# Optimization experiments

Measured on AMD Instinct MI355X. Metric: run time of the kernel, lower is better.

The kernel has to match this reference:

```python
import jax, jax.numpy as jnp
import numpy as np

MEAN = np.array([0.485, 0.456, 0.406], np.float32).reshape(1, 3, 1, 1)
STD = np.array([0.229, 0.224, 0.225], np.float32).reshape(1, 3, 1, 1)
BN_EPS = 1e-5


def _srm_kernels():
    """Standard SRM 30-filter 5x5 high-pass bank (Fridrich) -> [30,1,5,5]."""
    ks = []
    Z = lambda: np.zeros((5, 5), np.float32)
    D8 = [(-1, 0), (-1, 1), (0, 1), (1, 1), (1, 0), (1, -1), (0, -1), (-1, -1)]
    for dy, dx in D8:  # 8 first-order
        k = Z(); k[2, 2] = -1.0; k[2 + dy, 2 + dx] = 1.0; ks.append(k)
    for dy, dx in D8[:4]:  # 4 second-order
        k = Z(); k[2, 2] = -2.0; k[2 + dy, 2 + dx] = 1.0; k[2 - dy, 2 - dx] = 1.0
        ks.append(k / 2.0)
    for dy, dx in D8:  # 8 third-order
        k = Z()
        k[2 - dy, 2 - dx] = -1.0; k[2, 2] = 3.0
        k[2 + dy, 2 + dx] = -3.0; k[2 + 2 * dy, 2 + 2 * dx] = 1.0
        ks.append(k / 3.0)
    sq3 = np.array([[-1, 2, -1], [2, -4, 2], [-1, 2, -1]], np.float32) / 4.0
    k = Z(); k[1:4, 1:4] = sq3; ks.append(k)  # SQUARE 3x3
    sq5 = np.array([[-1, 2, -2, 2, -1], [2, -6, 8, -6, 2], [-2, 8, -12, 8, -2],
                    [2, -6, 8, -6, 2], [-1, 2, -2, 2, -1]], np.float32) / 12.0
    ks.append(sq5)  # SQUARE 5x5
    e3 = np.array([[-1, 2, -1], [2, -4, 2], [0, 0, 0]], np.float32) / 4.0
    for r in range(4):  # 4 EDGE 3x3
        k = Z(); k[1:4, 1:4] = np.rot90(e3, r); ks.append(k)
    e5 = np.array([[-1, 2, -2, 2, -1], [2, -6, 8, -6, 2], [-2, 8, -12, 8, -2],
                   [0, 0, 0, 0, 0], [0, 0, 0, 0, 0]], np.float32) / 4.0
    for r in range(4):  # 4 EDGE 5x5
        ks.append(np.rot90(e5, r).copy())
    return np.stack(ks)[:, None]  # [30,1,5,5]

SRM_K = jnp.asarray(_srm_kernels())
GAUSS_K = jnp.asarray((np.outer([1, 4, 6, 4, 1], [1, 4, 6, 4, 1]) / 256.0)
                      .astype(np.float32))[None, None]  # [1,1,5,5]
CFA_K = jnp.asarray((np.array([[0, 1, 0], [1, 0, 1], [0, 1, 0]], np.float32) / 4.0))[None, None]


def conv2d(x, w, b=None):
    y = jax.lax.conv_general_dilated(x, w, (1, 1), 'SAME',
                                     dimension_numbers=('NCHW', 'OIHW', 'NCHW'))
    if b is not None:
        y = y + b[None, :, None, None]
    return y


def batchnorm(x, g, b, m, v):
    inv = jax.lax.rsqrt(v + BN_EPS)
    return (x - m[None, :, None, None]) * (g * inv)[None, :, None, None] + b[None, :, None, None]


def extract_features(x):
    """Batched PRNU(1) + SRM(30) + CFA(1) feature maps -> [B,32,H,W]."""
    img = jnp.clip(x * STD + MEAN, 0.0, 1.0)  # denormalize
    gray = (0.299 * img[:, 0] + 0.587 * img[:, 1] + 0.114 * img[:, 2])[:, None]  # [B,1,H,W]
    prnu = gray - conv2d(gray, GAUSS_K)            # denoise-subtract noise residual
    srm = conv2d(gray, SRM_K)                       # [B,30,H,W]
    green = img[:, 1:2]
    cfa = green - conv2d(green, CFA_K)              # CFA interpolation residual
    return jnp.concatenate([prnu, srm, cfa], axis=1)  # [B,32,H,W]


def setup_inputs() -> dict:
    key = jax.random.key(0)
    ks = jax.random.split(key, 16)
    B, H, W = 16, 256, 256
    d = {"x": jax.random.normal(ks[0], (B, 3, H, W), jnp.float32)}
    cins = [32, 64, 64, 64]
    for i in range(4):
        cin, co = cins[i], 64
        scale = (2.0 / (cin * 9)) ** 0.5  # kaiming
        d[f"w{i+1}"] = jax.random.normal(ks[1 + i], (co, cin, 3, 3), jnp.float32) * scale
        d[f"b{i+1}"] = jnp.zeros((co,), jnp.float32)
        d[f"g{i+1}"] = jnp.ones((co,), jnp.float32)
        d[f"be{i+1}"] = jnp.zeros((co,), jnp.float32)
        d[f"m{i+1}"] = jax.random.normal(ks[5 + i], (co,), jnp.float32) * 0.1
        d[f"v{i+1}"] = jax.random.uniform(ks[9 + i], (co,), jnp.float32, 0.5, 1.5)
    return d


def reference(x, w1, b1, g1, be1, m1, v1, w2, b2, g2, be2, m2, v2,
              w3, b3, g3, be3, m3, v3, w4, b4, g4, be4, m4, v4):
    h = extract_features(x)
    for w, b, g, be, m, v in ((w1, b1, g1, be1, m1, v1), (w2, b2, g2, be2, m2, v2),
                              (w3, b3, g3, be3, m3, v3), (w4, b4, g4, be4, m4, v4)):
        h = jax.nn.relu(batchnorm(conv2d(h, w, b), g, be, m, v))
    return h  # [B,64,H,W]
```

## Files before the change

### kernel.cpp

```cpp
#include <hip/hip_runtime.h>
#include <hip/hip_bf16.h>
#include <cstddef>

#define B_ 16
#define H_ 256
#define W_ 256
#define HW_ (H_ * W_)
#define P_ 258


typedef _Float16 half8 __attribute__((ext_vector_type(8)));
typedef float floatx4 __attribute__((ext_vector_type(4)));

__device__ __forceinline__ void gload_lds16(void* lds, const void* g) {
  __builtin_amdgcn_global_load_lds(
      (const __attribute__((address_space(1))) unsigned int*)g,
      (__attribute__((address_space(3))) unsigned int*)lds, 16, 0, 0);
}

__global__ __launch_bounds__(256) void zero_border3(_Float16* __restrict__ f,
                                                    _Float16* __restrict__ a,
                                                    _Float16* __restrict__ bb) {
  int idx = blockIdx.x * 256 + threadIdx.x;
  int total = 16 * 20 * 1028;
  if (idx >= total) return;
  int p = idx % 1028;
  int rest = idx / 1028;
  int cg = rest % 20;
  int b = rest / 20;
  _Float16* buf;
  int ncg, c;
  if (cg < 4) { buf = f; ncg = 4; c = cg; }
  else if (cg < 12) { buf = a; ncg = 8; c = cg - 4; }
  else { buf = bb; ncg = 8; c = cg - 12; }
  int row, col;
  if (p < 258) { row = 0; col = p; }
  else if (p < 516) { row = 257; col = p - 258; }
  else if (p < 772) { row = p - 515; col = 0; }
  else { row = p - 771; col = 257; }
  *(floatx4*)&buf[(((size_t)(b * ncg + c) * P_ + row) * P_ + col) * 8] =
      (floatx4)0.f;
}

__global__ __launch_bounds__(256) void feat_kernel(const float* __restrict__ x,
                                                   _Float16* __restrict__ F) {
  __shared__ float sg[36][37];
  __shared__ float sgr[36][37];

  const int b = blockIdx.z;
  const int y0 = blockIdx.y * 32;
  const int x0 = blockIdx.x * 32;
  const float* xb = x + (size_t)b * 3 * HW_;

  for (int i = threadIdx.x; i < 36 * 36; i += 256) {
    int iy = i / 36, ix = i % 36;
    int gy = y0 + iy - 2, gx = x0 + ix - 2;
    float gray = 0.f, green = 0.f;
    if (gy >= 0 && gy < H_ && gx >= 0 && gx < W_) {
      int idx = gy * W_ + gx;
      float r = fminf(fmaxf(xb[idx] * 0.229f + 0.485f, 0.f), 1.f);
      float g = fminf(fmaxf(xb[idx + HW_] * 0.224f + 0.456f, 0.f), 1.f);
      float bl = fminf(fmaxf(xb[idx + 2 * HW_] * 0.225f + 0.406f, 0.f), 1.f);
      gray = 0.299f * r + 0.587f * g + 0.114f * bl;
      green = g;
    }
    sg[iy][ix] = gray;
    sgr[iy][ix] = green;
  }
  __syncthreads();

  for (int p = threadIdx.x; p < 32 * 32; p += 256) {
    const int py = p >> 5, px = p & 31;
    const int ly = py + 2, lx = px + 2;
#define G(dy, dx) sg[ly + (dy)][lx + (dx)]
    float f[32];
    const float c = G(0, 0);

    {
      const float ga[5] = {1.f, 4.f, 6.f, 4.f, 1.f};
      float s = 0.f;
#pragma unroll
      for (int i = 0; i < 5; i++) {
        float rs = 0.f;
#pragma unroll
        for (int j = 0; j < 5; j++) rs += ga[j] * G(i - 2, j - 2);
        s += ga[i] * rs;
      }
      f[0] = c - s * (1.0f / 256.0f);
    }

    const int dy8[8] = {-1, -1, 0, 1, 1, 1, 0, -1};
    const int dx8[8] = {0, 1, 1, 1, 0, -1, -1, -1};

#pragma unroll
    for (int k = 0; k < 8; k++) f[1 + k] = G(dy8[k], dx8[k]) - c;
#pragma unroll
    for (int k = 0; k < 4; k++)
      f[9 + k] = 0.5f * (G(dy8[k], dx8[k]) + G(-dy8[k], -dx8[k])) - c;
#pragma unroll
    for (int k = 0; k < 8; k++)
      f[13 + k] = (-G(-dy8[k], -dx8[k]) + 3.f * c - 3.f * G(dy8[k], dx8[k]) +
                   G(2 * dy8[k], 2 * dx8[k])) * (1.f / 3.f);

    {
      const float sq3[3][3] = {{-1, 2, -1}, {2, -4, 2}, {-1, 2, -1}};
      float s = 0.f;
#pragma unroll
      for (int i = 0; i < 3; i++)
#pragma unroll
        for (int j = 0; j < 3; j++) s += sq3[i][j] * G(i - 1, j - 1);
      f[21] = s * 0.25f;
    }
    {
      const float sq5[5][5] = {{-1, 2, -2, 2, -1},
                               {2, -6, 8, -6, 2},
                               {-2, 8, -12, 8, -2},
                               {2, -6, 8, -6, 2},
                               {-1, 2, -2, 2, -1}};
      float s = 0.f;
#pragma unroll
      for (int i = 0; i < 5; i++)
#pragma unroll
        for (int j = 0; j < 5; j++) s += sq5[i][j] * G(i - 2, j - 2);
      f[22] = s * (1.0f / 12.0f);
    }
    {
      const float e3[3][3] = {{-1, 2, -1}, {2, -4, 2}, {0, 0, 0}};
      float s0 = 0.f, s1 = 0.f, s2 = 0.f, s3 = 0.f;
#pragma unroll
      for (int i = 0; i < 3; i++)
#pragma unroll
        for (int j = 0; j < 3; j++) {
          float v = G(i - 1, j - 1);
          s0 += e3[i][j] * v;
          s1 += e3[j][2 - i] * v;
          s2 += e3[2 - i][2 - j] * v;
          s3 += e3[2 - j][i] * v;
        }
      f[23] = s0 * 0.25f;
      f[24] = s1 * 0.25f;
      f[25] = s2 * 0.25f;
      f[26] = s3 * 0.25f;
    }
    {
      const float e5[5][5] = {{-1, 2, -2, 2, -1},
                              {2, -6, 8, -6, 2},
                              {-2, 8, -12, 8, -2},
                              {0, 0, 0, 0, 0},
                              {0, 0, 0, 0, 0}};
      float s0 = 0.f, s1 = 0.f, s2 = 0.f, s3 = 0.f;
#pragma unroll
      for (int i = 0; i < 5; i++)
#pragma unroll
        for (int j = 0; j < 5; j++) {
          float v = G(i - 2, j - 2);
          s0 += e5[i][j] * v;
          s1 += e5[j][4 - i] * v;
          s2 += e5[4 - i][4 - j] * v;
          s3 += e5[4 - j][i] * v;
        }
      f[27] = s0 * 0.25f;
      f[28] = s1 * 0.25f;
      f[29] = s2 * 0.25f;
      f[30] = s3 * 0.25f;
    }
    {
      float gc = sgr[ly][lx];
      f[31] = gc - 0.25f * (sgr[ly - 1][lx] + sgr[ly][lx - 1] +
                            sgr[ly][lx + 1] + sgr[ly + 1][lx]);
    }
#undef G

    _Float16 h[32];
#pragma unroll
    for (int cc = 0; cc < 32; cc++) h[cc] = (_Float16)f[cc];
    const floatx4* src = (const floatx4*)h;
#pragma unroll
    for (int cg = 0; cg < 4; cg++)
      *(floatx4*)&F[(((size_t)(b * 4 + cg) * P_ + (y0 + py + 1)) * P_ +
                     (x0 + px + 1)) * 8] = src[cg];
  }
}

__global__ void wprep4_kernel(
    const float* __restrict__ w1, const float* __restrict__ b1,
    const float* __restrict__ g1, const float* __restrict__ be1,
    const float* __restrict__ m1, const float* __restrict__ v1,
    const float* __restrict__ w2, const float* __restrict__ b2,
    const float* __restrict__ g2, const float* __restrict__ be2,
    const float* __restrict__ m2, const float* __restrict__ v2,
    const float* __restrict__ w3, const float* __restrict__ b3,
    const float* __restrict__ g3, const float* __restrict__ be3,
    const float* __restrict__ m3, const float* __restrict__ v3,
    const float* __restrict__ w4, const float* __restrict__ b4,
    const float* __restrict__ g4, const float* __restrict__ be4,
    const float* __restrict__ m4, const float* __restrict__ v4,
    _Float16* __restrict__ wp1, _Float16* __restrict__ wp2,
    _Float16* __restrict__ wp3, _Float16* __restrict__ wp4,
    float* __restrict__ scsh) {
  const int layer = blockIdx.y;
  const float *w, *bias, *g, *be, *m, *v;
  _Float16* wp;
  int cin;
  switch (layer) {
    case 0: w = w1; bias = b1; g = g1; be = be1; m = m1; v = v1; wp = wp1; cin = 32; break;
    case 1: w = w2; bias = b2; g = g2; be = be2; m = m2; v = v2; wp = wp2; cin = 64; break;
    case 2: w = w3; bias = b3; g = g3; be = be3; m = m3; v = v3; wp = wp3; cin = 64; break;
    default: w = w4; bias = b4; g = g4; be = be4; m = m4; v = v4; wp = wp4; cin = 64; break;
  }
  int i = blockIdx.x * 256 + threadIdx.x;
  int total = cin * 9 * 64;
  if (i < total) {
    int j = i & 7;
    int co = (i >> 3) & 63;
    int rest = i >> 9;
    int t = rest % 9;
    int qc = rest / 9;
    int ci = qc * 8 + j;
    wp[i] = (_Float16)w[((size_t)co * cin + ci) * 9 + t];
  }
  if (i < 64) {
    float s = g[i] * rsqrtf(v[i] + 1e-5f);
    scsh[layer * 128 + i] = s;
    scsh[layer * 128 + 64 + i] = be[i] + (bias[i] - m[i]) * s;
  }
}

template <int CIN, bool FINAL>
__global__ __launch_bounds__(256, 2) void conv_mfma(
    const _Float16* __restrict__ in, const _Float16* __restrict__ wp,
    const float* __restrict__ sc, const float* __restrict__ sh,
    void* __restrict__ outv) {
  __shared__ char smem[42240];
  _Float16(*s_in)[10][66][8] = (_Float16(*)[10][66][8])smem;

  const int tid = threadIdx.x;
  const int b = blockIdx.z;
  const int y0 = blockIdx.y * 8;
  const int x0 = blockIdx.x * 64;
  const int wid = tid >> 6;
  const int lane = tid & 63;
  const int quad = lane >> 4;
  const int ln = lane & 15;

  floatx4 acc[8][4];
#pragma unroll
  for (int mt = 0; mt < 8; mt++)
#pragma unroll
    for (int nt = 0; nt < 4; nt++) acc[mt][nt] = (floatx4)0.f;

  for (int kc = 0; kc < CIN / 32; kc++) {
    __syncthreads();
    for (int i = tid; i < 2640; i += 256) {
      int q = i / 660, rem = i % 660;
      int row = rem / 66, col = rem % 66;
      gload_lds16(smem + i * 16,
                  &in[(((size_t)(b * (CIN / 8) + kc * 4 + q) * P_ +
                        (y0 + row)) * P_ + (x0 + col)) * 8]);
    }
    __syncthreads();

    const _Float16* wq = wp + (size_t)(kc * 4 + quad) * 9 * 512;
#pragma unroll
    for (int t = 0; t < 9; t++) {
      const int ty = t / 3, tx = t % 3;
      half8 a[8], bb[4];
#pragma unroll
      for (int nt = 0; nt < 4; nt++)
        bb[nt] = *(const half8*)&wq[t * 512 + (nt * 16 + ln) * 8];
#pragma unroll
      for (int mt = 0; mt < 8; mt++)
        a[mt] = *(const half8*)&s_in[quad][2 * wid + ty + (mt >> 2)]
                                    [(mt & 3) * 16 + ln + tx][0];
#pragma unroll
      for (int mt = 0; mt < 8; mt++)
#pragma unroll
        for (int nt = 0; nt < 4; nt++)
          acc[mt][nt] = __builtin_amdgcn_mfma_f32_16x16x32_f16(
              a[mt], bb[nt], acc[mt][nt], 0, 0, 0);
    }
  }

  if (FINAL) {
    float* out = (float*)outv;
#pragma unroll
    for (int nt = 0; nt < 4; nt++) {
      int co = nt * 16 + ln;
      float s = sc[co], t0 = sh[co];
#pragma unroll
      for (int mt = 0; mt < 8; mt++) {
        int y = y0 + 2 * wid + (mt >> 2);
        int xb = x0 + (mt & 3) * 16 + quad * 4;
        floatx4 vv;
#pragma unroll
        for (int r = 0; r < 4; r++) vv[r] = fmaxf(acc[mt][nt][r] * s + t0, 0.f);
        *(floatx4*)&out[(((size_t)b * 64 + co) * H_ + y) * W_ + xb] = vv;
      }
    }
  } else {
    __syncthreads();
    _Float16* s_out = (_Float16*)smem + wid * 5280;
    _Float16* out = (_Float16*)outv;
#pragma unroll
    for (int h = 0; h < 2; h++) {
      asm volatile("s_waitcnt lgkmcnt(0)" ::: "memory");
#pragma unroll
      for (int nt = 0; nt < 4; nt++) {
        int co = nt * 16 + ln;
        float s = sc[co], t0 = sh[co];
        int cog = co >> 3, clo = co & 7;
#pragma unroll
        for (int mt2 = 0; mt2 < 4; mt2++) {
          int lpix0 = mt2 * 16 + quad * 4;
#pragma unroll
          for (int r = 0; r < 4; r++) {
            int lpix = lpix0 + r;
            s_out[lpix * 64 + (((cog ^ (lpix & 7)) << 3) | clo)] =
                (_Float16)fmaxf(acc[h * 4 + mt2][nt][r] * s + t0, 0.f);
          }
        }
      }
      asm volatile("s_waitcnt lgkmcnt(0)" ::: "memory");
      int gy = y0 + 2 * wid + h + 1;
#pragma unroll
      for (int cog = 0; cog < 8; cog++) {
        *(floatx4*)&out[(((size_t)(b * 8 + cog) * P_ + gy) * P_ +
                         (x0 + lane + 1)) * 8] =
            *(const floatx4*)&s_out[lane * 64 + ((cog ^ (lane & 7)) << 3)];
      }
    }
  }
}

extern "C" void kernel_launch(void* const* d_in, const int* in_sizes, int n_in,
                              void* d_out, int out_size, void* d_ws,
                              size_t ws_size, hipStream_t stream) {
  const float* x = (const float*)d_in[0];
#define LAYER_PTRS(i)                                                       \
  const float* w##i = (const float*)d_in[1 + ((i)-1) * 6 + 0];              \
  const float* b##i = (const float*)d_in[1 + ((i)-1) * 6 + 1];              \
  const float* g##i = (const float*)d_in[1 + ((i)-1) * 6 + 2];              \
  const float* be##i = (const float*)d_in[1 + ((i)-1) * 6 + 3];             \
  const float* m##i = (const float*)d_in[1 + ((i)-1) * 6 + 4];              \
  const float* v##i = (const float*)d_in[1 + ((i)-1) * 6 + 5];
  LAYER_PTRS(1)
  LAYER_PTRS(2)
  LAYER_PTRS(3)
  LAYER_PTRS(4)
#undef LAYER_PTRS

  char* ws = (char*)d_ws;
  const size_t featB = (size_t)16 * 4 * P_ * P_ * 8 * 2;
  const size_t actB64 = (size_t)16 * 8 * P_ * P_ * 8 * 2;
  _Float16* feat = (_Float16*)ws;
  _Float16* actA = (_Float16*)(ws + featB);
  _Float16* actB = (_Float16*)(ws + featB + actB64);
  char* wbase = ws + featB + 2 * actB64;
  _Float16* wp1 = (_Float16*)(wbase);
  _Float16* wp2 = (_Float16*)(wbase + 36864);
  _Float16* wp3 = (_Float16*)(wbase + 36864 + 73728);
  _Float16* wp4 = (_Float16*)(wbase + 36864 + 2 * 73728);
  float* scsh = (float*)(wbase + 36864 + 3 * 73728);
  float *sc1 = scsh, *sh1 = scsh + 64;
  float *sc2 = scsh + 128, *sh2 = scsh + 192;
  float *sc3 = scsh + 256, *sh3 = scsh + 320;
  float *sc4 = scsh + 384, *sh4 = scsh + 448;

  dim3 wgrid(144, 4);
  wprep4_kernel<<<wgrid, 256, 0, stream>>>(
      w1, b1, g1, be1, m1, v1, w2, b2, g2, be2, m2, v2,
      w3, b3, g3, be3, m3, v3, w4, b4, g4, be4, m4, v4,
      wp1, wp2, wp3, wp4, scsh);

  zero_border3<<<1285, 256, 0, stream>>>(feat, actA, actB);

  dim3 fgrid(W_ / 32, H_ / 32, B_);
  feat_kernel<<<fgrid, 256, 0, stream>>>(x, feat);

  dim3 cgrid(W_ / 64, H_ / 8, B_);
  conv_mfma<32, false><<<cgrid, 256, 0, stream>>>(feat, wp1, sc1, sh1, actA);
  conv_mfma<64, false><<<cgrid, 256, 0, stream>>>(actA, wp2, sc2, sh2, actB);
  conv_mfma<64, false><<<cgrid, 256, 0, stream>>>(actB, wp3, sc3, sh3, actA);
  conv_mfma<64, true><<<cgrid, 256, 0, stream>>>(actA, wp4, sc4, sh4, d_out);
}
```

Measured before the change: 696.9 us.

## Double-buffer conv input tiles, retile to 16x32, prefetch weights and swizzle block order

The 3x3 MFMA conv kernel now uses 16x32-pixel tiles instead of 8x64, which shrinks halo overhead. Input channel chunks are staged into double-buffered LDS, so the next chunk's global-to-LDS copy overlaps the current chunk's MFMAs. Weights are repacked into a lane-contiguous layout and software-prefetched two taps ahead in alternating registers. A 1D grid with a remapped block index groups spatially neighbouring tiles across XCDs. The cost is more LDS per block (two buffers for the 64-channel layers), which may reduce occupancy.

```diff
diff --git a/kernel.cpp b/kernel.cpp
--- a/kernel.cpp
+++ b/kernel.cpp
@@ -212,11 +212,14 @@
   int total = cin * 9 * 64;
   if (i < total) {
     int j = i & 7;
-    int co = (i >> 3) & 63;
-    int rest = i >> 9;
+    int ln = (i >> 3) & 15;
+    int quad = (i >> 7) & 3;
+    int nt = (i >> 9) & 3;
+    int rest = i >> 11;
     int t = rest % 9;
-    int qc = rest / 9;
-    int ci = qc * 8 + j;
+    int kc = rest / 9;
+    int ci = (kc * 4 + quad) * 8 + j;
+    int co = nt * 16 + ln;
     wp[i] = (_Float16)w[((size_t)co * cin + ci) * 9 + t];
   }
   if (i < 64) {
@@ -231,13 +234,18 @@
     const _Float16* __restrict__ in, const _Float16* __restrict__ wp,
     const float* __restrict__ sc, const float* __restrict__ sh,
     void* __restrict__ outv) {
-  __shared__ char smem[42240];
-  _Float16(*s_in)[10][66][8] = (_Float16(*)[10][66][8])smem;
+  constexpr int NP = CIN / 8;
+  constexpr int NKC = CIN / 32;
+  constexpr int IN_BYTES = 4 * 18 * 34 * 8 * 2;
+  __shared__ char smem[NKC * IN_BYTES];
+
+  const int bid = blockIdx.x;
+  const int sid = (bid & 7) * 256 + (bid >> 3);
+  const int b = sid >> 7;
+  const int y0 = ((sid >> 3) & 15) * 16;
+  const int x0 = (sid & 7) * 32;
 
   const int tid = threadIdx.x;
-  const int b = blockIdx.z;
-  const int y0 = blockIdx.y * 8;
-  const int x0 = blockIdx.x * 64;
   const int wid = tid >> 6;
   const int lane = tid & 63;
   const int quad = lane >> 4;
@@ -249,36 +257,62 @@
 #pragma unroll
     for (int nt = 0; nt < 4; nt++) acc[mt][nt] = (floatx4)0.f;
 
-  for (int kc = 0; kc < CIN / 32; kc++) {
-    __syncthreads();
-    for (int i = tid; i < 2640; i += 256) {
-      int q = i / 660, rem = i % 660;
-      int row = rem / 66, col = rem % 66;
-      gload_lds16(smem + i * 16,
-                  &in[(((size_t)(b * (CIN / 8) + kc * 4 + q) * P_ +
-                        (y0 + row)) * P_ + (x0 + col)) * 8]);
-    }
-    __syncthreads();
-
-    const _Float16* wq = wp + (size_t)(kc * 4 + quad) * 9 * 512;
+  auto stage = [&](int bufidx, int kcn) {
+    char* dst = smem + bufidx * IN_BYTES;
+    for (int i = tid; i < 2448; i += 256) {
+      int q = i / 612, rem = i % 612;
+      int row = rem / 34, col = rem % 34;
+      gload_lds16(dst + i * 16,
+                  &in[(((size_t)(b * NP + kcn * 4 + q) * P_ + (y0 + row)) * P_ +
+                       (x0 + col)) * 8]);
+    }
+  };
+
+  const _Float16* wl = wp + (size_t)lane * 8;
+#define LOADW(dst, g)                                                   \
+  {                                                                     \
+    _Pragma("unroll") for (int nt_ = 0; nt_ < 4; nt_++) dst[nt_] =      \
+        *(const half8*)&wl[(size_t)((g) * 4 + nt_) * 512];              \
+  }
+
+  stage(0, 0);
+  __syncthreads();
+
+  for (int kc = 0; kc < NKC; kc++) {
+    if (kc + 1 < NKC) stage((kc + 1) & 1, kc + 1);
+    const _Float16* si = (const _Float16*)(smem + (kc & 1) * IN_BYTES);
+
+    half8 bbA[4], bbB[4];
+    const int g0 = kc * 9;
+    LOADW(bbA, g0 + 0)
+    LOADW(bbB, g0 + 1)
 #pragma unroll
     for (int t = 0; t < 9; t++) {
       const int ty = t / 3, tx = t % 3;
-      half8 a[8], bb[4];
-#pragma unroll
-      for (int nt = 0; nt < 4; nt++)
-        bb[nt] = *(const half8*)&wq[t * 512 + (nt * 16 + ln) * 8];
+      half8 a[8];
 #pragma unroll
       for (int mt = 0; mt < 8; mt++)
-        a[mt] = *(const half8*)&s_in[quad][2 * wid + ty + (mt >> 2)]
-                                    [(mt & 3) * 16 + ln + tx][0];
-#pragma unroll
-      for (int mt = 0; mt < 8; mt++)
-#pragma unroll
-        for (int nt = 0; nt < 4; nt++)
-          acc[mt][nt] = __builtin_amdgcn_mfma_f32_16x16x32_f16(
-              a[mt], bb[nt], acc[mt][nt], 0, 0, 0);
-    }
+        a[mt] = *(const half8*)&si[(((quad * 18 + 4 * wid + (mt >> 1) + ty) *
+                                    34) + (mt & 1) * 16 + ln + tx) * 8];
+      if ((t & 1) == 0) {
+#pragma unroll
+        for (int mt = 0; mt < 8; mt++)
+#pragma unroll
+          for (int nt = 0; nt < 4; nt++)
+            acc[mt][nt] = __builtin_amdgcn_mfma_f32_16x16x32_f16(
+                a[mt], bbA[nt], acc[mt][nt], 0, 0, 0);
+        if (t + 2 < 9) LOADW(bbA, g0 + t + 2)
+      } else {
+#pragma unroll
+        for (int mt = 0; mt < 8; mt++)
+#pragma unroll
+          for (int nt = 0; nt < 4; nt++)
+            acc[mt][nt] = __builtin_amdgcn_mfma_f32_16x16x32_f16(
+                a[mt], bbB[nt], acc[mt][nt], 0, 0, 0);
+        if (t + 2 < 9) LOADW(bbB, g0 + t + 2)
+      }
+    }
+    __syncthreads();
   }
 
   if (FINAL) {
@@ -289,8 +323,8 @@
       float s = sc[co], t0 = sh[co];
 #pragma unroll
       for (int mt = 0; mt < 8; mt++) {
-        int y = y0 + 2 * wid + (mt >> 2);
-        int xb = x0 + (mt & 3) * 16 + quad * 4;
+        int y = y0 + 4 * wid + (mt >> 1);
+        int xb = x0 + (mt & 1) * 16 + quad * 4;
         floatx4 vv;
 #pragma unroll
         for (int r = 0; r < 4; r++) vv[r] = fmaxf(acc[mt][nt][r] * s + t0, 0.f);
@@ -298,8 +332,7 @@
       }
     }
   } else {
-    __syncthreads();
-    _Float16* s_out = (_Float16*)smem + wid * 5280;
+    _Float16* s_out = (_Float16*)smem + wid * 4096;
     _Float16* out = (_Float16*)outv;
 #pragma unroll
     for (int h = 0; h < 2; h++) {
@@ -321,15 +354,16 @@
         }
       }
       asm volatile("s_waitcnt lgkmcnt(0)" ::: "memory");
-      int gy = y0 + 2 * wid + h + 1;
+      int gy = y0 + 4 * wid + 2 * h + (lane >> 5) + 1;
+      int gx = x0 + (lane & 31) + 1;
 #pragma unroll
       for (int cog = 0; cog < 8; cog++) {
-        *(floatx4*)&out[(((size_t)(b * 8 + cog) * P_ + gy) * P_ +
-                         (x0 + lane + 1)) * 8] =
+        *(floatx4*)&out[(((size_t)(b * 8 + cog) * P_ + gy) * P_ + gx) * 8] =
             *(const floatx4*)&s_out[lane * 64 + ((cog ^ (lane & 7)) << 3)];
       }
     }
   }
+#undef LOADW
 }
 
 extern "C" void kernel_launch(void* const* d_in, const int* in_sizes, int n_in,
@@ -377,9 +411,8 @@
   dim3 fgrid(W_ / 32, H_ / 32, B_);
   feat_kernel<<<fgrid, 256, 0, stream>>>(x, feat);
 
-  dim3 cgrid(W_ / 64, H_ / 8, B_);
-  conv_mfma<32, false><<<cgrid, 256, 0, stream>>>(feat, wp1, sc1, sh1, actA);
-  conv_mfma<64, false><<<cgrid, 256, 0, stream>>>(actA, wp2, sc2, sh2, actB);
-  conv_mfma<64, false><<<cgrid, 256, 0, stream>>>(actB, wp3, sc3, sh3, actA);
-  conv_mfma<64, true><<<cgrid, 256, 0, stream>>>(actA, wp4, sc4, sh4, d_out);
-}
+  conv_mfma<32, false><<<2048, 256, 0, stream>>>(feat, wp1, sc1, sh1, actA);
+  conv_mfma<64, false><<<2048, 256, 0, stream>>>(actA, wp2, sc2, sh2, actB);
+  conv_mfma<64, false><<<2048, 256, 0, stream>>>(actB, wp3, sc3, sh3, actA);
+  conv_mfma<64, true><<<2048, 256, 0, stream>>>(actA, wp4, sc4, sh4, d_out);
+}
```

Measured after the change: 708.5 us. Within noise of the previous version (+1.7%).
